# Kernel tuning notes

Hardware: AMD Instinct MI355X
Metric: run time of the kernel (lower is better)

The kernel has to match this reference:

```python
import jax, jax.numpy as jnp
import numpy as np

N_NEIGHBORS = 5
N_AUG = 1  # n_augmentations


def setup_inputs() -> dict:
    key = jax.random.key(0)
    x = jax.random.normal(key, (8192, 256), dtype=jnp.float32)
    return {"x": x}


def reference(x):
    # x: [N, d]
    N = x.shape[0]
    k = N_NEIGHBORS

    # All-pairs squared Euclidean distances (sklearn NearestNeighbors semantics)
    sq = jnp.sum(x * x, axis=1)                      # [N]
    dist = sq[:, None] + sq[None, :] - 2.0 * (x @ x.T)  # [N, N]

    # k+1 nearest (incl. self), drop self (column 0, distance 0)
    _, idx = jax.lax.top_k(-dist, k + 1)             # [N, k+1]
    nbrs = idx[:, 1:]                                # [N, k]

    # Original torch code picks a random permutation of the k neighbors and uses
    # only the first one (neighbor_idx[0]) with a random alpha per sample.
    # Equivalent: uniform random choice among k neighbors + uniform alpha.
    rng = jax.random.key(42)
    new_rows = []
    for a in range(N_AUG):
        kc, ka = jax.random.split(jax.random.fold_in(rng, a))
        choice = jax.random.randint(kc, (N,), 0, k)          # [N]
        alpha = jax.random.uniform(ka, (N, 1), dtype=x.dtype)  # [N, 1]
        sel = nbrs[jnp.arange(N), choice]                    # [N]
        new_rows.append((1.0 - alpha) * x + alpha * x[sel])  # [N, d]

    return jnp.concatenate([x] + new_rows, axis=0)  # [N*(1+N_AUG), d]
```

## Files before the change

### kernel.cpp

```cpp
#include <hip/hip_runtime.h>
#include <stdint.h>


#define NROWS 8192
#define ND4   64

typedef __attribute__((ext_vector_type(8))) short bf16x8;
typedef __attribute__((ext_vector_type(4))) float f32x4;

__device__ __forceinline__ uint32_t umin32(uint32_t a, uint32_t b) { return a < b ? a : b; }
__device__ __forceinline__ uint32_t umax32(uint32_t a, uint32_t b) { return a > b ? a : b; }

__device__ __forceinline__ uint32_t pkmin16(uint32_t a, uint32_t b) {
  uint32_t r;
  asm("v_pk_min_u16 %0, %1, %2" : "=v"(r) : "v"(a), "v"(b));
  return r;
}
__device__ __forceinline__ uint32_t pkmax16(uint32_t a, uint32_t b) {
  uint32_t r;
  asm("v_pk_max_u16 %0, %1, %2" : "=v"(r) : "v"(a), "v"(b));
  return r;
}

__device__ __forceinline__ uint32_t rotl32(uint32_t v, int d) {
  return (v << d) | (v >> (32 - d));
}

#define TFBODY(k0, k1)                                                        \
  const uint32_t ks2 = (k0) ^ (k1) ^ 0x1BD11BDAu;                             \
  x0 += (k0); x1 += (k1);                                                     \
  TFR(13) TFR(15) TFR(26) TFR(6)                                              \
  x0 += (k1);  x1 += ks2 + 1u;                                                \
  TFR(17) TFR(29) TFR(16) TFR(24)                                             \
  x0 += ks2; x1 += (k0) + 2u;                                                 \
  TFR(13) TFR(15) TFR(26) TFR(6)                                              \
  x0 += (k0);  x1 += (k1) + 3u;                                               \
  TFR(17) TFR(29) TFR(16) TFR(24)                                             \
  x0 += (k1);  x1 += ks2 + 4u;                                                \
  TFR(13) TFR(15) TFR(26) TFR(6)                                              \
  x0 += ks2; x1 += (k0) + 5u;

__device__ __forceinline__ void tf2x32(uint32_t k0, uint32_t k1,
                                       uint32_t& x0, uint32_t& x1) {
#define TFR(R) { x0 += x1; x1 = rotl32(x1, R); x1 ^= x0; }
  TFBODY(k0, k1)
#undef TFR
}

struct U2 { uint32_t x, y; };
constexpr uint32_t crotl(uint32_t v, int d) {
  return (v << d) | (v >> (32 - d));
}
constexpr U2 tfc(uint32_t k0, uint32_t k1, uint32_t x0, uint32_t x1) {
#define TFR(R) { x0 += x1; x1 = crotl(x1, R); x1 ^= x0; }
  TFBODY(k0, k1)
#undef TFR
  return U2{x0, x1};
}
constexpr U2 RG = tfc(0u, 42u, 0u, 0u);
constexpr U2 KC = tfc(RG.x, RG.y, 0u, 0u);
constexpr U2 KA = tfc(RG.x, RG.y, 0u, 1u);
constexpr U2 K1 = tfc(KC.x, KC.y, 0u, 0u);
constexpr U2 K2 = tfc(KC.x, KC.y, 0u, 1u);

__device__ __forceinline__ bool lessp(float a, int ai, float b, int bi) {
  return (a < b) || ((a == b) && (ai < bi));
}

__device__ __forceinline__ void insert6(float key, int idx,
                                        float (&v)[6], int (&ix)[6]) {
  if (!lessp(key, idx, v[5], ix[5])) return;
#pragma unroll
  for (int j = 5; j >= 1; --j) {
    if (lessp(key, idx, v[j - 1], ix[j - 1])) {
      v[j] = v[j - 1]; ix[j] = ix[j - 1];
    } else {
      v[j] = key; ix[j] = idx; return;
    }
  }
  v[0] = key; ix[0] = idx;
}

__device__ __forceinline__ unsigned short f2bf(float f) {
  uint32_t u = __float_as_uint(f);
  u += 0x7FFFu + ((u >> 16) & 1u);
  return (unsigned short)(u >> 16);
}

__device__ __forceinline__ void gload_lds16(const void* g, void* l) {
  __builtin_amdgcn_global_load_lds(
      (const __attribute__((address_space(1))) unsigned int*)g,
      (__attribute__((address_space(3))) unsigned int*)l, 16, 0, 0);
}

__global__ void prep_kernel(const float* __restrict__ x,
                            float* __restrict__ sq,
                            unsigned short* __restrict__ xbf) {
  int row  = blockIdx.x * 4 + (threadIdx.x >> 6);
  int lane = threadIdx.x & 63;
  const float4* xv4 = reinterpret_cast<const float4*>(x);
  float4 vv = xv4[(size_t)row * ND4 + lane];
  float t = vv.x * vv.x + vv.y * vv.y + vv.z * vv.z + vv.w * vv.w;
#pragma unroll
  for (int off = 32; off >= 1; off >>= 1) t += __shfl_down(t, off);
  if (lane == 0) sq[row] = t;
  ushort4 st;
  st.x = f2bf(vv.x); st.y = f2bf(vv.y); st.z = f2bf(vv.z); st.w = f2bf(vv.w);
  int T = row >> 5, h = (row >> 4) & 1, c = row & 15;
  int kb = lane >> 3, g = (lane >> 1) & 3, half8 = lane & 1;
  size_t f = ((size_t)(T * 8 + kb) * 2 + h) * 64 + g * 16 + c;
  *reinterpret_cast<ushort4*>(xbf + f * 8 + half8 * 4) = st;
}

__global__ __launch_bounds__(512, 4)
void gemm_topk_kernel(const unsigned short* __restrict__ xbf,
                      const float* __restrict__ sq,
                      uint32_t* __restrict__ cand) {
  __shared__ __align__(16) char smem[65664];
  uint32_t* skeys = reinterpret_cast<uint32_t*>(smem + 32768);

  const int tid = threadIdx.x;
  const int bid = blockIdx.x;
  const int rowblk = bid & 31;
  const int chunk  = bid >> 5;
  const int rowbase = rowblk * 256;
  const int colbase = chunk * 512;
  const int w = tid >> 6;
  const int l = tid & 63;
  const int c = l & 15;

  const uint4* xf4 = reinterpret_cast<const uint4*>(xbf);
  uint4 afr[16];
#pragma unroll
  for (int m = 0; m < 2; ++m)
#pragma unroll
    for (int kb = 0; kb < 8; ++kb)
      afr[m * 8 + kb] =
          xf4[((size_t)((rowblk * 8 + w) * 8 + kb) * 2 + m) * 64 + l];

  uint32_t v[6];
#pragma unroll
  for (int j = 0; j < 6; ++j) v[j] = 0xFFFFFFFFu;
  const int srow = tid >> 1, shalf = tid & 1;

  const char* xb = reinterpret_cast<const char*>(xbf);
#pragma unroll
  for (int i = 0; i < 2; ++i) {
    int p = i * 512 + tid;
    gload_lds16(xb + (size_t)(chunk * 16) * 16384 + p * 16, smem + p * 16);
  }
  __syncthreads();

  int buf = 0, kbf = 0;
  for (int tc = 0; tc < 16; ++tc) {
    if (tc < 15) {
#pragma unroll
      for (int i = 0; i < 2; ++i) {
        int p = i * 512 + tid;
        gload_lds16(xb + (size_t)(chunk * 16 + tc + 1) * 16384 + p * 16,
                    smem + (buf ^ 1) * 16384 + p * 16);
      }
    }
    float sqjq0 = sq[colbase + tc * 32 + c] * 0.25f;
    float sqjq1 = sq[colbase + tc * 32 + 16 + c] * 0.25f;

    f32x4 acc[2][2];
#pragma unroll
    for (int m = 0; m < 2; ++m)
#pragma unroll
      for (int n = 0; n < 2; ++n) acc[m][n] = (f32x4){0.f, 0.f, 0.f, 0.f};

    const char* Bb = smem + buf * 16384;
#pragma unroll
    for (int kb = 0; kb < 8; ++kb) {
      bf16x8 b[2];
#pragma unroll
      for (int n = 0; n < 2; ++n)
        b[n] = *reinterpret_cast<const bf16x8*>(
            Bb + kb * 2048 + n * 1024 + l * 16);
#pragma unroll
      for (int m = 0; m < 2; ++m) {
        bf16x8 av = __builtin_bit_cast(bf16x8, afr[m * 8 + kb]);
#pragma unroll
        for (int n = 0; n < 2; ++n)
          acc[m][n] = __builtin_amdgcn_mfma_f32_16x16x32_bf16(av, b[n], acc[m][n], 0, 0, 0);
      }
    }
    {
      const int g = l >> 4;
      const uint32_t meta = (uint32_t)((tc << 4) | c);
      uint32_t* sk = skeys + kbf * 4112 + c * 257;
#pragma unroll
      for (int m = 0; m < 2; ++m)
#pragma unroll
        for (int e = 0; e < 4; ++e) {
          float a0 = fmaf(acc[m][0][e], -0.5f, sqjq0);
          float a1 = fmaf(acc[m][1][e], -0.5f, sqjq1);
          uint32_t k0 = ((uint32_t)fmaxf(a0, 0.0f) << 8) | meta;
          uint32_t k1 = ((uint32_t)fmaxf(a1, 0.0f) << 8) | meta;
          uint32_t pk = (umin32(k1, 65535u) << 16) | umin32(k0, 65535u);
          sk[w * 32 + m * 16 + g * 4 + e] = pk;
        }
    }
    __syncthreads();
    {
      const uint32_t* sk = skeys + kbf * 4112;
#pragma unroll
      for (int u = 0; u < 8; ++u) {
        uint32_t t = sk[(shalf * 8 + u) * 257 + srow];
#pragma unroll
        for (int j = 0; j < 6; ++j) {
          uint32_t vj = v[j];
          v[j] = pkmin16(vj, t);
          t    = pkmax16(vj, t);
        }
      }
    }
    buf ^= 1; kbf ^= 1;
  }
  uint32_t fin[6];
#pragma unroll
  for (int j = 0; j < 6; ++j) fin[j] = 0xFFFFFFFFu;
#pragma unroll
  for (int j = 0; j < 6; ++j) {
    uint32_t p = v[j];
#pragma unroll
    for (int h = 0; h < 2; ++h) {
      uint32_t k16 = (h ? (p >> 16) : p) & 0xFFFFu;
      uint32_t ku = ((k16 >> 8) << 9) | ((k16 & 0xF0u) << 1) |
                    ((uint32_t)h << 4) | (k16 & 0xFu);
#pragma unroll
      for (int q = 0; q < 6; ++q) {
        uint32_t fq = fin[q];
        fin[q] = umin32(fq, ku);
        ku     = umax32(fq, ku);
      }
    }
  }
#pragma unroll
  for (int j = 0; j < 6; ++j) {
    uint32_t k = fin[j];
    cand[(size_t)(rowbase + srow) * 192 + chunk * 12 + shalf * 6 + j] =
        ((k >> 9) << 13) | (uint32_t)colbase | (k & 0x1FFu);
  }
}

__global__ __launch_bounds__(256)
void rescore_emit_kernel(const float* __restrict__ x,
                         const float* __restrict__ sq,
                         const uint32_t* __restrict__ cand,
                         float* __restrict__ out) {
  const int tid = threadIdx.x;
  const int wid = tid >> 6;
  const int l   = tid & 63;
  const int row = blockIdx.x * 4 + wid;

  uint32_t k0 = cand[(size_t)row * 192 + l];
  uint32_t k1 = cand[(size_t)row * 192 + 64 + l];
  uint32_t k2 = cand[(size_t)row * 192 + 128 + l];
  int mycol = row;
#pragma unroll
  for (int it = 0; it < 16; ++it) {
    uint32_t mv = umin32(k0, umin32(k1, k2));
#pragma unroll
    for (int off = 1; off < 64; off <<= 1) {
      uint32_t o = __shfl_xor(mv, off);
      mv = umin32(mv, o);
    }
    if (l == it) mycol = (int)(mv & 8191u);
    if (k0 == mv) k0 = 0xFFFFFFFFu;
    else if (k1 == mv) k1 = 0xFFFFFFFFu;
    else if (k2 == mv) k2 = 0xFFFFFFFFu;
  }

  const float4* x4 = reinterpret_cast<const float4*>(x);
  const int jg = l >> 2, dq = l & 3;
  const int cj = __shfl(mycol, jg);
  float acc = 0.0f;
#pragma unroll 4
  for (int i = 0; i < 16; ++i) {
    int d4 = i * 4 + dq;
    float4 a = x4[(size_t)row * 64 + d4];
    float4 b = x4[(size_t)cj * 64 + d4];
    acc = fmaf(a.x, b.x, acc);
    acc = fmaf(a.y, b.y, acc);
    acc = fmaf(a.z, b.z, acc);
    acc = fmaf(a.w, b.w, acc);
  }
  acc += __shfl_xor(acc, 1);
  acc += __shfl_xor(acc, 2);
  float myscore = sq[row] + sq[cj] - 2.0f * acc;

  float v6[6]; int i6[6];
#pragma unroll
  for (int j = 0; j < 6; ++j) { v6[j] = 3.402823466e38f; i6[j] = 0x7fffffff; }
#pragma unroll
  for (int j = 0; j < 16; ++j) {
    float scj = __shfl(myscore, j * 4);
    int   ccj = __shfl(mycol, j);
    insert6(scj, ccj, v6, i6);
  }

  uint32_t ri = (uint32_t)row;
  uint32_t h0 = 0, h1 = ri; tf2x32(K1.x, K1.y, h0, h1); uint32_t hb = h0 ^ h1;
  uint32_t l0 = 0, l1 = ri; tf2x32(K2.x, K2.y, l0, l1); uint32_t lb = l0 ^ l1;
  uint32_t u0 = 0, u1 = ri; tf2x32(KA.x, KA.y, u0, u1); uint32_t ub = u0 ^ u1;

  uint32_t ch = (hb % 5u + lb % 5u) % 5u;
  float al = __uint_as_float((ub >> 9) | 0x3F800000u) - 1.0f;
  al = fmaxf(0.0f, al);

  int sl = i6[1];
  sl = (ch == 1u) ? i6[2] : sl;
  sl = (ch == 2u) ? i6[3] : sl;
  sl = (ch == 3u) ? i6[4] : sl;
  sl = (ch == 4u) ? i6[5] : sl;

  float4 xi = x4[(size_t)row * 64 + l];
  float4 xs = x4[(size_t)sl * 64 + l];
  float om = 1.0f - al;
  float4 o;
  o.x = __fadd_rn(__fmul_rn(om, xi.x), __fmul_rn(al, xs.x));
  o.y = __fadd_rn(__fmul_rn(om, xi.y), __fmul_rn(al, xs.y));
  o.z = __fadd_rn(__fmul_rn(om, xi.z), __fmul_rn(al, xs.z));
  o.w = __fadd_rn(__fmul_rn(om, xi.w), __fmul_rn(al, xs.w));
  float4* out4 = reinterpret_cast<float4*>(out);
  out4[(size_t)row * 64 + l] = xi;
  out4[(size_t)(NROWS + row) * 64 + l] = o;
}

extern "C" void kernel_launch(void* const* d_in, const int* in_sizes, int n_in,
                              void* d_out, int out_size, void* d_ws, size_t ws_size,
                              hipStream_t stream) {
  const float* x = (const float*)d_in[0];
  float* out = (float*)d_out;
  char* ws = (char*)d_ws;

  float* sq = (float*)ws;
  unsigned short* xbf = (unsigned short*)(ws + 32768);
  uint32_t* cand = (uint32_t*)(ws + 32768 + 4194304);

  hipLaunchKernelGGL(prep_kernel,         dim3(2048), dim3(256), 0, stream, x, sq, xbf);
  hipLaunchKernelGGL(gemm_topk_kernel,    dim3(512),  dim3(512), 0, stream, xbf, sq, cand);
  hipLaunchKernelGGL(rescore_emit_kernel, dim3(2048), dim3(256), 0, stream, x, sq, cand, out);
}
```

Measured before the change: 73.14 us.

## Give each wave 64 rows and each thread a full row in GEMM top-k

```diff
diff --git a/kernel.cpp b/kernel.cpp
--- a/kernel.cpp
+++ b/kernel.cpp
@@ -112,11 +112,11 @@
   *reinterpret_cast<ushort4*>(xbf + f * 8 + half8 * 4) = st;
 }
 
-__global__ __launch_bounds__(512, 4)
+__global__ __launch_bounds__(256, 2)
 void gemm_topk_kernel(const unsigned short* __restrict__ xbf,
                       const float* __restrict__ sq,
                       uint32_t* __restrict__ cand) {
-  __shared__ __align__(16) char smem[65664];
+  __shared__ __align__(16) char smem[49216];
   uint32_t* skeys = reinterpret_cast<uint32_t*>(smem + 32768);
 
   const int tid = threadIdx.x;
@@ -127,36 +127,36 @@
   const int colbase = chunk * 512;
   const int w = tid >> 6;
   const int l = tid & 63;
+  const int g = l >> 4;
   const int c = l & 15;
 
   const uint4* xf4 = reinterpret_cast<const uint4*>(xbf);
-  uint4 afr[16];
-#pragma unroll
-  for (int m = 0; m < 2; ++m)
+  uint4 afr[32];
+#pragma unroll
+  for (int m = 0; m < 4; ++m)
 #pragma unroll
     for (int kb = 0; kb < 8; ++kb)
       afr[m * 8 + kb] =
-          xf4[((size_t)((rowblk * 8 + w) * 8 + kb) * 2 + m) * 64 + l];
+          xf4[((size_t)((rowblk * 8 + w * 2 + (m >> 1)) * 8 + kb) * 2 + (m & 1)) * 64 + l];
 
   uint32_t v[6];
 #pragma unroll
   for (int j = 0; j < 6; ++j) v[j] = 0xFFFFFFFFu;
-  const int srow = tid >> 1, shalf = tid & 1;
 
   const char* xb = reinterpret_cast<const char*>(xbf);
 #pragma unroll
-  for (int i = 0; i < 2; ++i) {
-    int p = i * 512 + tid;
+  for (int i = 0; i < 4; ++i) {
+    int p = i * 256 + tid;
     gload_lds16(xb + (size_t)(chunk * 16) * 16384 + p * 16, smem + p * 16);
   }
   __syncthreads();
 
-  int buf = 0, kbf = 0;
+  int buf = 0;
   for (int tc = 0; tc < 16; ++tc) {
     if (tc < 15) {
 #pragma unroll
-      for (int i = 0; i < 2; ++i) {
-        int p = i * 512 + tid;
+      for (int i = 0; i < 4; ++i) {
+        int p = i * 256 + tid;
         gload_lds16(xb + (size_t)(chunk * 16 + tc + 1) * 16384 + p * 16,
                     smem + (buf ^ 1) * 16384 + p * 16);
       }
@@ -164,34 +164,29 @@
     float sqjq0 = sq[colbase + tc * 32 + c] * 0.25f;
     float sqjq1 = sq[colbase + tc * 32 + 16 + c] * 0.25f;
 
-    f32x4 acc[2][2];
-#pragma unroll
-    for (int m = 0; m < 2; ++m)
+    f32x4 acc[4][2];
+#pragma unroll
+    for (int m = 0; m < 4; ++m)
 #pragma unroll
       for (int n = 0; n < 2; ++n) acc[m][n] = (f32x4){0.f, 0.f, 0.f, 0.f};
 
     const char* Bb = smem + buf * 16384;
 #pragma unroll
     for (int kb = 0; kb < 8; ++kb) {
-      bf16x8 b[2];
-#pragma unroll
-      for (int n = 0; n < 2; ++n)
-        b[n] = *reinterpret_cast<const bf16x8*>(
-            Bb + kb * 2048 + n * 1024 + l * 16);
-#pragma unroll
-      for (int m = 0; m < 2; ++m) {
+      bf16x8 b0 = *reinterpret_cast<const bf16x8*>(Bb + kb * 2048 + l * 16);
+      bf16x8 b1 = *reinterpret_cast<const bf16x8*>(Bb + kb * 2048 + 1024 + l * 16);
+#pragma unroll
+      for (int m = 0; m < 4; ++m) {
         bf16x8 av = __builtin_bit_cast(bf16x8, afr[m * 8 + kb]);
-#pragma unroll
-        for (int n = 0; n < 2; ++n)
-          acc[m][n] = __builtin_amdgcn_mfma_f32_16x16x32_bf16(av, b[n], acc[m][n], 0, 0, 0);
+        acc[m][0] = __builtin_amdgcn_mfma_f32_16x16x32_bf16(av, b0, acc[m][0], 0, 0, 0);
+        acc[m][1] = __builtin_amdgcn_mfma_f32_16x16x32_bf16(av, b1, acc[m][1], 0, 0, 0);
       }
     }
     {
-      const int g = l >> 4;
       const uint32_t meta = (uint32_t)((tc << 4) | c);
-      uint32_t* sk = skeys + kbf * 4112 + c * 257;
-#pragma unroll
-      for (int m = 0; m < 2; ++m)
+      uint32_t* sk = skeys + c * 257 + w * 64 + g * 4;
+#pragma unroll
+      for (int m = 0; m < 4; ++m)
 #pragma unroll
         for (int e = 0; e < 4; ++e) {
           float a0 = fmaf(acc[m][0][e], -0.5f, sqjq0);
@@ -199,24 +194,21 @@
           uint32_t k0 = ((uint32_t)fmaxf(a0, 0.0f) << 8) | meta;
           uint32_t k1 = ((uint32_t)fmaxf(a1, 0.0f) << 8) | meta;
           uint32_t pk = (umin32(k1, 65535u) << 16) | umin32(k0, 65535u);
-          sk[w * 32 + m * 16 + g * 4 + e] = pk;
+          sk[m * 16 + e] = pk;
         }
     }
+#pragma unroll
+    for (int pc = 0; pc < 16; ++pc) {
+      uint32_t t = skeys[pc * 257 + tid];
+#pragma unroll
+      for (int j = 0; j < 6; ++j) {
+        uint32_t vj = v[j];
+        v[j] = pkmin16(vj, t);
+        t    = pkmax16(vj, t);
+      }
+    }
     __syncthreads();
-    {
-      const uint32_t* sk = skeys + kbf * 4112;
-#pragma unroll
-      for (int u = 0; u < 8; ++u) {
-        uint32_t t = sk[(shalf * 8 + u) * 257 + srow];
-#pragma unroll
-        for (int j = 0; j < 6; ++j) {
-          uint32_t vj = v[j];
-          v[j] = pkmin16(vj, t);
-          t    = pkmax16(vj, t);
-        }
-      }
-    }
-    buf ^= 1; kbf ^= 1;
+    buf ^= 1;
   }
   uint32_t fin[6];
 #pragma unroll
@@ -240,7 +232,7 @@
 #pragma unroll
   for (int j = 0; j < 6; ++j) {
     uint32_t k = fin[j];
-    cand[(size_t)(rowbase + srow) * 192 + chunk * 12 + shalf * 6 + j] =
+    cand[(size_t)(rowbase + tid) * 96 + chunk * 6 + j] =
         ((k >> 9) << 13) | (uint32_t)colbase | (k & 0x1FFu);
   }
 }
@@ -255,13 +247,12 @@
   const int l   = tid & 63;
   const int row = blockIdx.x * 4 + wid;
 
-  uint32_t k0 = cand[(size_t)row * 192 + l];
-  uint32_t k1 = cand[(size_t)row * 192 + 64 + l];
-  uint32_t k2 = cand[(size_t)row * 192 + 128 + l];
+  uint32_t k0 = cand[(size_t)row * 96 + l];
+  uint32_t k1 = (l < 32) ? cand[(size_t)row * 96 + 64 + l] : 0xFFFFFFFFu;
   int mycol = row;
 #pragma unroll
   for (int it = 0; it < 16; ++it) {
-    uint32_t mv = umin32(k0, umin32(k1, k2));
+    uint32_t mv = umin32(k0, k1);
 #pragma unroll
     for (int off = 1; off < 64; off <<= 1) {
       uint32_t o = __shfl_xor(mv, off);
@@ -270,7 +261,6 @@
     if (l == it) mycol = (int)(mv & 8191u);
     if (k0 == mv) k0 = 0xFFFFFFFFu;
     else if (k1 == mv) k1 = 0xFFFFFFFFu;
-    else if (k2 == mv) k2 = 0xFFFFFFFFu;
   }
 
   const float4* x4 = reinterpret_cast<const float4*>(x);
@@ -341,6 +331,6 @@
   uint32_t* cand = (uint32_t*)(ws + 32768 + 4194304);
 
   hipLaunchKernelGGL(prep_kernel,         dim3(2048), dim3(256), 0, stream, x, sq, xbf);
-  hipLaunchKernelGGL(gemm_topk_kernel,    dim3(512),  dim3(512), 0, stream, xbf, sq, cand);
+  hipLaunchKernelGGL(gemm_topk_kernel,    dim3(512),  dim3(256), 0, stream, xbf, sq, cand);
   hipLaunchKernelGGL(rescore_emit_kernel, dim3(2048), dim3(256), 0, stream, x, sq, cand, out);
 }
```

After: 76.63 us. 1.05x slower.

## Halve column chunk per block, single-buffer key LDS, merge halves via shuffle

Applied to the files above, without the earlier changes.

```diff
diff --git a/kernel.cpp b/kernel.cpp
--- a/kernel.cpp
+++ b/kernel.cpp
@@ -112,11 +112,11 @@
   *reinterpret_cast<ushort4*>(xbf + f * 8 + half8 * 4) = st;
 }
 
-__global__ __launch_bounds__(512, 4)
+__global__ __launch_bounds__(512, 6)
 void gemm_topk_kernel(const unsigned short* __restrict__ xbf,
                       const float* __restrict__ sq,
                       uint32_t* __restrict__ cand) {
-  __shared__ __align__(16) char smem[65664];
+  __shared__ __align__(16) char smem[49216];
   uint32_t* skeys = reinterpret_cast<uint32_t*>(smem + 32768);
 
   const int tid = threadIdx.x;
@@ -124,9 +124,10 @@
   const int rowblk = bid & 31;
   const int chunk  = bid >> 5;
   const int rowbase = rowblk * 256;
-  const int colbase = chunk * 512;
+  const int colbase = chunk * 256;
   const int w = tid >> 6;
   const int l = tid & 63;
+  const int g = l >> 4;
   const int c = l & 15;
 
   const uint4* xf4 = reinterpret_cast<const uint4*>(xbf);
@@ -141,23 +142,24 @@
   uint32_t v[6];
 #pragma unroll
   for (int j = 0; j < 6; ++j) v[j] = 0xFFFFFFFFu;
-  const int srow = tid >> 1, shalf = tid & 1;
+  const int srowL = w * 32 + (l >> 1);
+  const int shalf = l & 1;
 
   const char* xb = reinterpret_cast<const char*>(xbf);
 #pragma unroll
   for (int i = 0; i < 2; ++i) {
     int p = i * 512 + tid;
-    gload_lds16(xb + (size_t)(chunk * 16) * 16384 + p * 16, smem + p * 16);
+    gload_lds16(xb + (size_t)(chunk * 8) * 16384 + p * 16, smem + p * 16);
   }
   __syncthreads();
 
-  int buf = 0, kbf = 0;
-  for (int tc = 0; tc < 16; ++tc) {
-    if (tc < 15) {
+  int buf = 0;
+  for (int tc = 0; tc < 8; ++tc) {
+    if (tc < 7) {
 #pragma unroll
       for (int i = 0; i < 2; ++i) {
         int p = i * 512 + tid;
-        gload_lds16(xb + (size_t)(chunk * 16 + tc + 1) * 16384 + p * 16,
+        gload_lds16(xb + (size_t)(chunk * 8 + tc + 1) * 16384 + p * 16,
                     smem + (buf ^ 1) * 16384 + p * 16);
       }
     }
@@ -173,23 +175,18 @@
     const char* Bb = smem + buf * 16384;
 #pragma unroll
     for (int kb = 0; kb < 8; ++kb) {
-      bf16x8 b[2];
-#pragma unroll
-      for (int n = 0; n < 2; ++n)
-        b[n] = *reinterpret_cast<const bf16x8*>(
-            Bb + kb * 2048 + n * 1024 + l * 16);
+      bf16x8 b0 = *reinterpret_cast<const bf16x8*>(Bb + kb * 2048 + l * 16);
+      bf16x8 b1 = *reinterpret_cast<const bf16x8*>(Bb + kb * 2048 + 1024 + l * 16);
 #pragma unroll
       for (int m = 0; m < 2; ++m) {
         bf16x8 av = __builtin_bit_cast(bf16x8, afr[m * 8 + kb]);
-#pragma unroll
-        for (int n = 0; n < 2; ++n)
-          acc[m][n] = __builtin_amdgcn_mfma_f32_16x16x32_bf16(av, b[n], acc[m][n], 0, 0, 0);
+        acc[m][0] = __builtin_amdgcn_mfma_f32_16x16x32_bf16(av, b0, acc[m][0], 0, 0, 0);
+        acc[m][1] = __builtin_amdgcn_mfma_f32_16x16x32_bf16(av, b1, acc[m][1], 0, 0, 0);
       }
     }
     {
-      const int g = l >> 4;
       const uint32_t meta = (uint32_t)((tc << 4) | c);
-      uint32_t* sk = skeys + kbf * 4112 + c * 257;
+      uint32_t* sk = skeys + c * 257 + w * 32 + g * 4;
 #pragma unroll
       for (int m = 0; m < 2; ++m)
 #pragma unroll
@@ -199,24 +196,21 @@
           uint32_t k0 = ((uint32_t)fmaxf(a0, 0.0f) << 8) | meta;
           uint32_t k1 = ((uint32_t)fmaxf(a1, 0.0f) << 8) | meta;
           uint32_t pk = (umin32(k1, 65535u) << 16) | umin32(k0, 65535u);
-          sk[w * 32 + m * 16 + g * 4 + e] = pk;
+          sk[m * 16 + e] = pk;
         }
     }
+#pragma unroll
+    for (int u = 0; u < 8; ++u) {
+      uint32_t t = skeys[(shalf * 8 + u) * 257 + srowL];
+#pragma unroll
+      for (int j = 0; j < 6; ++j) {
+        uint32_t vj = v[j];
+        v[j] = pkmin16(vj, t);
+        t    = pkmax16(vj, t);
+      }
+    }
     __syncthreads();
-    {
-      const uint32_t* sk = skeys + kbf * 4112;
-#pragma unroll
-      for (int u = 0; u < 8; ++u) {
-        uint32_t t = sk[(shalf * 8 + u) * 257 + srow];
-#pragma unroll
-        for (int j = 0; j < 6; ++j) {
-          uint32_t vj = v[j];
-          v[j] = pkmin16(vj, t);
-          t    = pkmax16(vj, t);
-        }
-      }
-    }
-    buf ^= 1; kbf ^= 1;
+    buf ^= 1;
   }
   uint32_t fin[6];
 #pragma unroll
@@ -237,11 +231,26 @@
       }
     }
   }
+  uint32_t oth[6];
+#pragma unroll
+  for (int j = 0; j < 6; ++j) oth[j] = __shfl_xor(fin[j], 1);
 #pragma unroll
   for (int j = 0; j < 6; ++j) {
-    uint32_t k = fin[j];
-    cand[(size_t)(rowbase + srow) * 192 + chunk * 12 + shalf * 6 + j] =
-        ((k >> 9) << 13) | (uint32_t)colbase | (k & 0x1FFu);
+    uint32_t t = oth[j];
+#pragma unroll
+    for (int q = 0; q < 6; ++q) {
+      uint32_t fq = fin[q];
+      fin[q] = umin32(fq, t);
+      t      = umax32(fq, t);
+    }
+  }
+  if (shalf == 0) {
+#pragma unroll
+    for (int j = 0; j < 6; ++j) {
+      uint32_t k = fin[j];
+      cand[(size_t)(rowbase + srowL) * 192 + chunk * 6 + j] =
+          ((k >> 9) << 13) | (uint32_t)colbase | (k & 0xFFu);
+    }
   }
 }
 
@@ -341,6 +350,6 @@
   uint32_t* cand = (uint32_t*)(ws + 32768 + 4194304);
 
   hipLaunchKernelGGL(prep_kernel,         dim3(2048), dim3(256), 0, stream, x, sq, xbf);
-  hipLaunchKernelGGL(gemm_topk_kernel,    dim3(512),  dim3(512), 0, stream, xbf, sq, cand);
+  hipLaunchKernelGGL(gemm_topk_kernel,    dim3(1024), dim3(512), 0, stream, xbf, sq, cand);
   hipLaunchKernelGGL(rescore_emit_kernel, dim3(2048), dim3(256), 0, stream, x, sq, cand, out);
 }
```

Measured after the change: 129.9 us. +77.7%, slower.
